# Performance work log

Measured on AMD Instinct MI355X. Metric: run time of the kernel, lower is better.

## Reference

```python
import jax, jax.numpy as jnp
import numpy as np

B, S, E, H = 8, 2048, 1024, 128  # batch, seq, emd_dim, head_size
DROP_P = 0.1


def setup_inputs() -> dict:
    key = jax.random.key(0)
    kx, ku, kq, kk, kv = jax.random.split(key, 5)
    x = jax.random.normal(kx, (B, S, E), dtype=jnp.float32)
    drop_u = jax.random.uniform(ku, (B, S, S), dtype=jnp.float32)
    # Linear(emd_dim, head_size, bias=False): store weights as [E, H] so y = x @ W
    scale = 1.0 / np.sqrt(E)
    wq = jax.random.uniform(kq, (E, H), dtype=jnp.float32, minval=-scale, maxval=scale)
    wk = jax.random.uniform(kk, (E, H), dtype=jnp.float32, minval=-scale, maxval=scale)
    wv = jax.random.uniform(kv, (E, H), dtype=jnp.float32, minval=-scale, maxval=scale)
    return {"x": x, "wq": wq, "wk": wk, "wv": wv, "drop_u": drop_u}


def reference(x, wq, wk, wv, drop_u):
    Edim = x.shape[-1]
    q = x @ wq  # [B,S,H]
    k = x @ wk
    v = x @ wv
    # NOTE: module scales by emd_dim**-0.5 (E), not head_size**-0.5
    att = jnp.einsum("bsh,bth->bst", q, k) * (Edim ** -0.5)
    att = jax.nn.softmax(att, axis=-1)
    # deterministic inverted dropout with p=0.1
    keep = (drop_u >= DROP_P).astype(att.dtype) / (1.0 - DROP_P)
    att = att * keep
    return jnp.einsum("bst,bth->bsh", att, v)
```

## Files before the change

### kernel.cpp

```cpp
#include <hip/hip_runtime.h>
#include <hip/hip_bf16.h>
#include <stdint.h>
#include <stddef.h>

#define B_ 8
#define S_ 2048
#define E_ 1024
#define H_ 128
#define NR_ (B_ * S_)

typedef __attribute__((ext_vector_type(8))) short short8;
typedef __attribute__((ext_vector_type(4))) short short4v;
typedef __attribute__((ext_vector_type(4))) float f32x4;

__device__ __forceinline__ short f2bf(float f){
  uint32_t u = __builtin_bit_cast(uint32_t, f);
  u = (u + 0x7FFFu + ((u >> 16) & 1u)) >> 16;
  return (short)(uint16_t)u;
}

#define GLOBAL_AS __attribute__((address_space(1)))
#define LDS_AS    __attribute__((address_space(3)))
__device__ __forceinline__ void async16(const void* g, void* l){
  __builtin_amdgcn_global_load_lds((const GLOBAL_AS uint32_t*)g,
                                   (LDS_AS uint32_t*)l, 16, 0, 0);
}

__global__ void prep(const float* __restrict__ x, const float* __restrict__ wq,
                     const float* __restrict__ wk, const float* __restrict__ wv,
                     short* __restrict__ xb, short* __restrict__ wt){
  __shared__ float t[32][33];
  int bid = blockIdx.x;
  if (bid < 8192){
    size_t i = ((size_t)bid * 256 + threadIdx.x) * 8;
    f32x4 a = *(const f32x4*)(x + i);
    f32x4 b = *(const f32x4*)(x + i + 4);
    short8 o;
#pragma unroll
    for (int j = 0; j < 4; j++){ o[j] = f2bf(a[j]); o[j + 4] = f2bf(b[j]); }
    *(short8*)(xb + i) = o;
  } else {
    int idx = bid - 8192;
    int hb  = idx & 3;
    int eb  = (idx >> 2) & 31;
    int w   = idx >> 7;
    const float* src = (w == 0) ? wq : (w == 1) ? wk : wv;
    int c  = threadIdx.x & 31;
    int r0 = threadIdx.x >> 5;
#pragma unroll
    for (int i = 0; i < 4; i++){
      int r = r0 * 4 + i;
      t[r][c] = src[(size_t)(eb * 32 + r) * H_ + hb * 32 + c];
    }
    __syncthreads();
#pragma unroll
    for (int i = 0; i < 4; i++){
      int r = r0 * 4 + i;
      wt[(size_t)(w * 128 + hb * 32 + r) * E_ + eb * 32 + c] = f2bf(t[c][r]);
    }
  }
}

__launch_bounds__(256)
__global__ void qkv_gemm(const short* __restrict__ xb, const short* __restrict__ wt,
                         short* __restrict__ qm, short* __restrict__ km,
                         short* __restrict__ vt){
  __shared__ __align__(16) short smem[16896];
  const int wave = threadIdx.x >> 6;
  const int lane = threadIdx.x & 63;
  const int l16  = lane & 15;
  const int quad = lane >> 4;
  const int nb   = blockIdx.x;
  const int m0   = blockIdx.y * 128;
  const int n0   = nb * 128;

  f32x4 acc[4][4];
#pragma unroll
  for (int i = 0; i < 4; i++)
#pragma unroll
    for (int j = 0; j < 4; j++) acc[i][j] = (f32x4)(0.0f);

#define STAGE(buf, k0)                                                        \
  {                                                                           \
    _Pragma("unroll")                                                         \
    for (int i = 0; i < 2; i++){                                              \
      int c = wave * 2 + i;                                                   \
      int r = c * 16 + (lane >> 2);                                           \
      int q = ((lane & 3) ^ ((r >> 1) & 3)) & 3;                              \
      async16(xb + (size_t)(m0 + r) * E_ + (k0) + q * 8,                      \
              (char*)(smem + (buf) * 4096) + c * 1024);                       \
      async16(wt + (size_t)(n0 + r) * E_ + (k0) + q * 8,                      \
              (char*)(smem + 8192 + (buf) * 4096) + c * 1024);                \
    }                                                                         \
  }

  STAGE(0, 0)
  for (int ks = 0; ks < 32; ks++){
    const int k0 = ks * 32;
    __syncthreads();
    if (ks < 31) STAGE((ks + 1) & 1, k0 + 32)

    const short* a = smem + (ks & 1) * 4096;
    const short* b = smem + 8192 + (ks & 1) * 4096;
    short8 af[4], bf[4];
#pragma unroll
    for (int t = 0; t < 4; t++){
      int ra = (wave & 1) * 64 + t * 16 + l16;
      int pa = (quad ^ ((ra >> 1) & 3)) & 3;
      af[t] = *(const short8*)(a + ra * 32 + pa * 8);
      int rb = (wave >> 1) * 64 + t * 16 + l16;
      int pb = (quad ^ ((rb >> 1) & 3)) & 3;
      bf[t] = *(const short8*)(b + rb * 32 + pb * 8);
    }
#pragma unroll
    for (int mt = 0; mt < 4; mt++)
#pragma unroll
      for (int nt = 0; nt < 4; nt++)
        acc[mt][nt] = __builtin_amdgcn_mfma_f32_16x16x32_bf16(af[mt], bf[nt], acc[mt][nt], 0, 0, 0);
  }
#undef STAGE

  if (nb != 2){
    short* dst = (nb == 0) ? qm : km;
#pragma unroll
    for (int mt = 0; mt < 4; mt++)
#pragma unroll
      for (int nt = 0; nt < 4; nt++){
        int row = m0 + (wave & 1) * 64 + mt * 16 + quad * 4;
        int col = (wave >> 1) * 64 + nt * 16 + l16;
#pragma unroll
        for (int r = 0; r < 4; r++)
          dst[(size_t)(row + r) * H_ + col] = f2bf(acc[mt][nt][r]);
      }
  } else {
    __syncthreads();
#pragma unroll
    for (int mt = 0; mt < 4; mt++)
#pragma unroll
      for (int nt = 0; nt < 4; nt++){
        int scol = (wave & 1) * 64 + mt * 16 + quad * 4;
        int hrow = (wave >> 1) * 64 + nt * 16 + l16;
        short4v t4;
#pragma unroll
        for (int r = 0; r < 4; r++) t4[r] = f2bf(acc[mt][nt][r]);
        *(short4v*)(smem + hrow * 132 + scol) = t4;
      }
    __syncthreads();
    int h   = threadIdx.x >> 1;
    int s0  = (threadIdx.x & 1) * 64;
    int bb_ = m0 >> 11;
    short* dstv = vt + ((size_t)bb_ * H_ + h) * S_ + (m0 & (S_ - 1)) + s0;
    const short* srcv = smem + h * 132 + s0;
#pragma unroll
    for (int i = 0; i < 8; i++)
      *(short8*)(dstv + i * 8) = *(const short8*)(srcv + i * 8);
  }
}

__launch_bounds__(512)
__global__ void attn(const short* __restrict__ qm, const short* __restrict__ km,
                     const short* __restrict__ vtm, const float* __restrict__ du,
                     float* __restrict__ po, float* __restrict__ pl,
                     float* __restrict__ out, int split){
  const int wave = threadIdx.x >> 6;
  const int lane = threadIdx.x & 63;
  const int l16  = lane & 15;
  const int quad = lane >> 4;
  const int sp   = blockIdx.x & (split - 1);
  const int rbk  = blockIdx.x / split;
  const int b    = rbk >> 4;
  const int m0   = (rbk & 15) * 128 + wave * 16;
  const int seg  = S_ / split;

  const short* qb  = qm  + ((size_t)b * S_ + m0) * H_;
  const short* kb  = km  + (size_t)b * S_ * H_;
  const short* vb  = vtm + (size_t)b * H_ * S_;
  const float* dub = du  + ((size_t)b * S_ + m0) * S_;

  __shared__ __align__(16) short kls[8192];
  __shared__ __align__(16) short vls[8192];
  __shared__ short pbuf[8][16][72];
  short* pb = &pbuf[wave][0][0];

  short8 qf[4];
#pragma unroll
  for (int kc = 0; kc < 4; kc++)
    qf[kc] = *(const short8*)(qb + (size_t)l16 * H_ + kc * 32 + quad * 8);

  f32x4 o[8];
#pragma unroll
  for (int ht = 0; ht < 8; ht++) o[ht] = (f32x4)(0.0f);
  float lpart[4] = {0.f, 0.f, 0.f, 0.f};

  const float SC2  = 0.045084220f;
  const float KINV = 1.0f / 0.9f;

  const int tbeg = sp * seg;
  for (int t0 = tbeg; t0 < tbeg + seg; t0 += 64){
#pragma unroll
    for (int i = 0; i < 2; i++){
      int c = wave * 2 + i;
      int r = c * 4 + (lane >> 4);
      int s = lane & 15;
      int q = (s & 8) | ((s ^ r) & 7);
      async16(kb + (size_t)(t0 + r) * H_ + q * 8, (char*)kls + c * 1024);
    }
#pragma unroll
    for (int i = 0; i < 2; i++){
      int c = wave * 2 + i;
      int r = c * 8 + (lane >> 3);
      int s = lane & 7;
      int q = (s ^ r) & 7;
      async16(vb + (size_t)r * S_ + t0 + q * 8, (char*)vls + c * 1024);
    }
    __syncthreads();

    const float* dp = dub + (size_t)l16 * S_ + t0 + quad * 8;
    f32x4 u0 = *(const f32x4*)(dp);
    f32x4 u1 = *(const f32x4*)(dp + 4);
    f32x4 u2 = *(const f32x4*)(dp + 32);
    f32x4 u3 = *(const f32x4*)(dp + 36);

    f32x4 s[4];
#pragma unroll
    for (int nt = 0; nt < 4; nt++) s[nt] = (f32x4)(0.0f);
#pragma unroll
    for (int nt = 0; nt < 4; nt++){
      int row = nt * 16 + l16;
#pragma unroll
      for (int kc = 0; kc < 4; kc++){
        int q  = kc * 4 + quad;
        int ph = (q & 8) | ((q ^ row) & 7);
        short8 bf = *(const short8*)((const char*)kls + row * 256 + ph * 16);
        s[nt] = __builtin_amdgcn_mfma_f32_16x16x32_bf16(qf[kc], bf, s[nt], 0, 0, 0);
      }
    }

#pragma unroll
    for (int nt = 0; nt < 4; nt++)
#pragma unroll
      for (int r = 0; r < 4; r++){
        float p = exp2f(s[nt][r] * SC2);
        lpart[r] += p;
        pb[(quad * 4 + r) * 72 + nt * 16 + l16] = f2bf(p);
      }

    __builtin_amdgcn_sched_barrier(0);
    __builtin_amdgcn_s_waitcnt(0xC07F);
    __builtin_amdgcn_sched_barrier(0);

    const short* pr = pb + l16 * 72 + quad * 8;
    short8 pb0 = *(const short8*)(pr);
    short8 pb1 = *(const short8*)(pr + 32);
    short8 pa0, pa1;
#pragma unroll
    for (int j = 0; j < 4; j++){
      pa0[j]     = (u0[j] >= 0.1f) ? pb0[j]     : (short)0;
      pa0[j + 4] = (u1[j] >= 0.1f) ? pb0[j + 4] : (short)0;
      pa1[j]     = (u2[j] >= 0.1f) ? pb1[j]     : (short)0;
      pa1[j + 4] = (u3[j] >= 0.1f) ? pb1[j + 4] : (short)0;
    }

#pragma unroll
    for (int ht = 0; ht < 8; ht++){
      int row = ht * 16 + l16;
#pragma unroll
      for (int half = 0; half < 2; half++){
        int q  = half * 4 + quad;
        int ph = (q ^ row) & 7;
        short8 vf = *(const short8*)((const char*)vls + row * 128 + ph * 16);
        o[ht] = __builtin_amdgcn_mfma_f32_16x16x32_bf16(half ? pa1 : pa0, vf, o[ht], 0, 0, 0);
      }
    }
    __syncthreads();
  }

  float lrow[4];
#pragma unroll
  for (int r = 0; r < 4; r++){
    float v = lpart[r];
    v += __shfl_xor(v, 1);
    v += __shfl_xor(v, 2);
    v += __shfl_xor(v, 4);
    v += __shfl_xor(v, 8);
    lrow[r] = v;
  }

  if (split == 1){
    float* op = out + ((size_t)b * S_ + m0) * H_;
#pragma unroll
    for (int ht = 0; ht < 8; ht++)
#pragma unroll
      for (int r = 0; r < 4; r++)
        op[(size_t)(quad * 4 + r) * H_ + ht * 16 + l16] = o[ht][r] * KINV / lrow[r];
  } else {
#pragma unroll
    for (int r = 0; r < 4; r++){
      size_t R = (size_t)b * S_ + m0 + quad * 4 + r;
#pragma unroll
      for (int ht = 0; ht < 8; ht++)
        po[((size_t)sp * NR_ + R) * H_ + ht * 16 + l16] = o[ht][r] * KINV;
      if (l16 == 0) pl[(size_t)sp * NR_ + R] = lrow[r];
    }
  }
}

__global__ void combine(const float* __restrict__ po, const float* __restrict__ pl,
                        float* __restrict__ out, int split){
  int row = blockIdx.x;
  int col = threadIdx.x;
  float num = 0.f, den = 0.f;
  for (int s = 0; s < split; s++){
    num += po[((size_t)s * NR_ + row) * H_ + col];
    den += pl[(size_t)s * NR_ + row];
  }
  out[(size_t)row * H_ + col] = num / den;
}

extern "C" void kernel_launch(void* const* d_in, const int* in_sizes, int n_in,
                              void* d_out, int out_size, void* d_ws, size_t ws_size,
                              hipStream_t stream){
  const float* x  = (const float*)d_in[0];
  const float* wq = (const float*)d_in[1];
  const float* wk = (const float*)d_in[2];
  const float* wv = (const float*)d_in[3];
  const float* du = (const float*)d_in[4];
  float* out = (float*)d_out;

  const size_t MiB = 1048576;
  char* ws = (char*)d_ws;
  short* qm = (short*)(ws);
  short* km = (short*)(ws + 4 * MiB);
  short* vt = (short*)(ws + 8 * MiB);
  short* xb = (short*)(ws + 12 * MiB);
  short* wt = (short*)(ws + 44 * MiB);
  float* pl = (float*)(ws + 45 * MiB);
  float* po = (float*)(ws + 45 * MiB + 524288);

  size_t base  = 45 * MiB + 524288;
  size_t needA = base + 32 * MiB;
  size_t needB = base + 16 * MiB;
  int split = (ws_size >= needA) ? 4 : (ws_size >= needB) ? 2 : 1;

  hipLaunchKernelGGL(prep,     dim3(8576),        dim3(256), 0, stream, x, wq, wk, wv, xb, wt);
  hipLaunchKernelGGL(qkv_gemm, dim3(3, 128),      dim3(256), 0, stream, xb, wt, qm, km, vt);
  hipLaunchKernelGGL(attn,     dim3(128 * split), dim3(512), 0, stream,
                     qm, km, vt, du, po, pl, out, split);
  if (split > 1)
    hipLaunchKernelGGL(combine, dim3(NR_), dim3(H_), 0, stream, po, pl, out, split);
}
```

Before: 290.5 us.

## Fuse fp32-to-bf16 conversion of x into QKV GEMM A-tile staging

Removes the separate pass that converted x to a bf16 workspace copy. The GEMM now loads fp32 x directly into registers, packs it to bf16 with the hardware packed-convert instruction, and writes it swizzled into LDS after the MFMA block, overlapping the global load with compute. This saves a 64 MiB read plus 32 MiB write plus re-read, but each GEMM block column reads x three times (once per Q/K/V tile) in fp32, and the A path is now register-staged rather than async.

```diff
diff --git a/kernel.cpp b/kernel.cpp
--- a/kernel.cpp
+++ b/kernel.cpp
@@ -19,6 +19,15 @@
   return (short)(uint16_t)u;
 }
 
+__device__ __forceinline__ short8 pack8(f32x4 a, f32x4 b){
+  union { short8 s; uint32_t u[4]; } r;
+  asm("v_cvt_pk_bf16_f32 %0, %1, %2" : "=v"(r.u[0]) : "v"(a[0]), "v"(a[1]));
+  asm("v_cvt_pk_bf16_f32 %0, %1, %2" : "=v"(r.u[1]) : "v"(a[2]), "v"(a[3]));
+  asm("v_cvt_pk_bf16_f32 %0, %1, %2" : "=v"(r.u[2]) : "v"(b[0]), "v"(b[1]));
+  asm("v_cvt_pk_bf16_f32 %0, %1, %2" : "=v"(r.u[3]) : "v"(b[2]), "v"(b[3]));
+  return r.s;
+}
+
 #define GLOBAL_AS __attribute__((address_space(1)))
 #define LDS_AS    __attribute__((address_space(3)))
 __device__ __forceinline__ void async16(const void* g, void* l){
@@ -26,43 +35,31 @@
                                    (LDS_AS uint32_t*)l, 16, 0, 0);
 }
 
-__global__ void prep(const float* __restrict__ x, const float* __restrict__ wq,
-                     const float* __restrict__ wk, const float* __restrict__ wv,
-                     short* __restrict__ xb, short* __restrict__ wt){
+__global__ void prep(const float* __restrict__ wq, const float* __restrict__ wk,
+                     const float* __restrict__ wv, short* __restrict__ wt){
   __shared__ float t[32][33];
-  int bid = blockIdx.x;
-  if (bid < 8192){
-    size_t i = ((size_t)bid * 256 + threadIdx.x) * 8;
-    f32x4 a = *(const f32x4*)(x + i);
-    f32x4 b = *(const f32x4*)(x + i + 4);
-    short8 o;
-#pragma unroll
-    for (int j = 0; j < 4; j++){ o[j] = f2bf(a[j]); o[j + 4] = f2bf(b[j]); }
-    *(short8*)(xb + i) = o;
-  } else {
-    int idx = bid - 8192;
-    int hb  = idx & 3;
-    int eb  = (idx >> 2) & 31;
-    int w   = idx >> 7;
-    const float* src = (w == 0) ? wq : (w == 1) ? wk : wv;
-    int c  = threadIdx.x & 31;
-    int r0 = threadIdx.x >> 5;
-#pragma unroll
-    for (int i = 0; i < 4; i++){
-      int r = r0 * 4 + i;
-      t[r][c] = src[(size_t)(eb * 32 + r) * H_ + hb * 32 + c];
-    }
-    __syncthreads();
-#pragma unroll
-    for (int i = 0; i < 4; i++){
-      int r = r0 * 4 + i;
-      wt[(size_t)(w * 128 + hb * 32 + r) * E_ + eb * 32 + c] = f2bf(t[c][r]);
-    }
+  int idx = blockIdx.x;
+  int hb  = idx & 3;
+  int eb  = (idx >> 2) & 31;
+  int w   = idx >> 7;
+  const float* src = (w == 0) ? wq : (w == 1) ? wk : wv;
+  int c  = threadIdx.x & 31;
+  int r0 = threadIdx.x >> 5;
+#pragma unroll
+  for (int i = 0; i < 4; i++){
+    int r = r0 * 4 + i;
+    t[r][c] = src[(size_t)(eb * 32 + r) * H_ + hb * 32 + c];
+  }
+  __syncthreads();
+#pragma unroll
+  for (int i = 0; i < 4; i++){
+    int r = r0 * 4 + i;
+    wt[(size_t)(w * 128 + hb * 32 + r) * E_ + eb * 32 + c] = f2bf(t[c][r]);
   }
 }
 
 __launch_bounds__(256)
-__global__ void qkv_gemm(const short* __restrict__ xb, const short* __restrict__ wt,
+__global__ void qkv_gemm(const float* __restrict__ x, const short* __restrict__ wt,
                          short* __restrict__ qm, short* __restrict__ km,
                          short* __restrict__ vt){
   __shared__ __align__(16) short smem[16896];
@@ -80,25 +77,56 @@
 #pragma unroll
     for (int j = 0; j < 4; j++) acc[i][j] = (f32x4)(0.0f);
 
-#define STAGE(buf, k0)                                                        \
+  int cA[2], rA[2], qA[2];
+#pragma unroll
+  for (int i = 0; i < 2; i++){
+    cA[i] = wave * 2 + i;
+    rA[i] = cA[i] * 16 + (lane >> 2);
+    qA[i] = ((lane & 3) ^ ((rA[i] >> 1) & 3)) & 3;
+  }
+
+  f32x4 a0[2], a1[2];
+
+#define A_LOAD(k0)                                                            \
+  {                                                                           \
+    _Pragma("unroll")                                                         \
+    for (int i = 0; i < 2; i++){                                              \
+      const float* s_ = x + (size_t)(m0 + rA[i]) * E_ + (k0) + qA[i] * 8;     \
+      a0[i] = *(const f32x4*)s_;                                              \
+      a1[i] = *(const f32x4*)(s_ + 4);                                        \
+    }                                                                         \
+  }
+
+#define A_WRITE(buf)                                                          \
+  {                                                                           \
+    _Pragma("unroll")                                                         \
+    for (int i = 0; i < 2; i++)                                               \
+      *(short8*)((char*)(smem + (buf) * 4096) + cA[i] * 1024 + lane * 16) =   \
+          pack8(a0[i], a1[i]);                                                \
+  }
+
+#define B_STAGE(buf, k0)                                                      \
   {                                                                           \
     _Pragma("unroll")                                                         \
     for (int i = 0; i < 2; i++){                                              \
       int c = wave * 2 + i;                                                   \
       int r = c * 16 + (lane >> 2);                                           \
       int q = ((lane & 3) ^ ((r >> 1) & 3)) & 3;                              \
-      async16(xb + (size_t)(m0 + r) * E_ + (k0) + q * 8,                      \
-              (char*)(smem + (buf) * 4096) + c * 1024);                       \
       async16(wt + (size_t)(n0 + r) * E_ + (k0) + q * 8,                      \
               (char*)(smem + 8192 + (buf) * 4096) + c * 1024);                \
     }                                                                         \
   }
 
-  STAGE(0, 0)
+  A_LOAD(0)
+  B_STAGE(0, 0)
+  A_WRITE(0)
   for (int ks = 0; ks < 32; ks++){
     const int k0 = ks * 32;
     __syncthreads();
-    if (ks < 31) STAGE((ks + 1) & 1, k0 + 32)
+    if (ks < 31){
+      A_LOAD(k0 + 32)
+      B_STAGE((ks + 1) & 1, k0 + 32)
+    }
 
     const short* a = smem + (ks & 1) * 4096;
     const short* b = smem + 8192 + (ks & 1) * 4096;
@@ -117,8 +145,14 @@
 #pragma unroll
       for (int nt = 0; nt < 4; nt++)
         acc[mt][nt] = __builtin_amdgcn_mfma_f32_16x16x32_bf16(af[mt], bf[nt], acc[mt][nt], 0, 0, 0);
-  }
-#undef STAGE
+
+    if (ks < 31){
+      A_WRITE((ks + 1) & 1)
+    }
+  }
+#undef A_LOAD
+#undef A_WRITE
+#undef B_STAGE
 
   if (nb != 2){
     short* dst = (nb == 0) ? qm : km;
@@ -332,7 +366,6 @@
   short* qm = (short*)(ws);
   short* km = (short*)(ws + 4 * MiB);
   short* vt = (short*)(ws + 8 * MiB);
-  short* xb = (short*)(ws + 12 * MiB);
   short* wt = (short*)(ws + 44 * MiB);
   float* pl = (float*)(ws + 45 * MiB);
   float* po = (float*)(ws + 45 * MiB + 524288);
@@ -342,8 +375,8 @@
   size_t needB = base + 16 * MiB;
   int split = (ws_size >= needA) ? 4 : (ws_size >= needB) ? 2 : 1;
 
-  hipLaunchKernelGGL(prep,     dim3(8576),        dim3(256), 0, stream, x, wq, wk, wv, xb, wt);
-  hipLaunchKernelGGL(qkv_gemm, dim3(3, 128),      dim3(256), 0, stream, xb, wt, qm, km, vt);
+  hipLaunchKernelGGL(prep,     dim3(384),         dim3(256), 0, stream, wq, wk, wv, wt);
+  hipLaunchKernelGGL(qkv_gemm, dim3(3, 128),      dim3(256), 0, stream, x, wt, qm, km, vt);
   hipLaunchKernelGGL(attn,     dim3(128 * split), dim3(512), 0, stream,
                      qm, km, vt, du, po, pl, out, split);
   if (split > 1)
```

New measurement: 293.3 us. About the same (+1.0%).
